# Optimization experiments

Hardware: AMD Instinct MI355X
Metric: run time of the kernel (lower is better)

## Reference

```python
import jax, jax.numpy as jnp
import numpy as np

F_NUM, KW, EMB = 256, 2, 300


def _conv_pool(X, W, b):
    # X: [B, L, E]; W: [F, kw, E]; b: [F]. Conv2d over [kw, E] window (full embedding
    # width) -> [B, F, T], ReLU, then AvgPool over the full T -> [B, F].
    kw = W.shape[1]
    T = X.shape[1] - kw + 1
    Xs = jnp.stack([X[:, k:k + T, :] for k in range(kw)], axis=1)  # [B, kw, T, E]
    y = jnp.einsum('fke,bkte->bft', W, Xs) + b[None, :, None]
    return jax.nn.relu(y).mean(axis=2)


def _unit(v):
    return v / jnp.sqrt((v * v).sum(-1, keepdims=True))


def setup_inputs() -> dict:
    key = jax.random.key(0)
    ks = jax.random.split(key, 20)
    wscale = 1.0 / np.sqrt(KW * EMB)
    inp = {
        'mention_vec': jax.random.normal(ks[0], (256, 10, 300), jnp.float32),
        'context_vec': jax.random.normal(ks[1], (256, 20, 300), jnp.float32),
        'doc_vec': jax.random.normal(ks[2], (200, 300), jnp.float32),
        'title_vec': jax.random.normal(ks[3], (1024, 20, 300), jnp.float32),
        'body_vec': jax.random.normal(ks[4], (1024, 200, 300), jnp.float32),
        'W_ms': jax.random.normal(ks[5], (F_NUM, KW, EMB), jnp.float32) * wscale,
        'b_ms': jax.random.normal(ks[6], (F_NUM,), jnp.float32) * wscale,
        'W_mc': jax.random.normal(ks[7], (F_NUM, KW, EMB), jnp.float32) * wscale,
        'b_mc': jax.random.normal(ks[8], (F_NUM,), jnp.float32) * wscale,
        'W_md': jax.random.normal(ks[9], (F_NUM, KW, EMB), jnp.float32) * wscale,
        'b_md': jax.random.normal(ks[10], (F_NUM,), jnp.float32) * wscale,
        'W_et': jax.random.normal(ks[11], (F_NUM, KW, EMB), jnp.float32) * wscale,
        'b_et': jax.random.normal(ks[12], (F_NUM,), jnp.float32) * wscale,
        'W_eb': jax.random.normal(ks[13], (F_NUM, KW, EMB), jnp.float32) * wscale,
        'b_eb': jax.random.normal(ks[14], (F_NUM,), jnp.float32) * wscale,
        'w_local': jax.random.normal(ks[15], (6,), jnp.float32) * 0.1,
        'b_local': jax.random.normal(ks[16], (1,), jnp.float32) * 0.1,
        'mention_entity': jax.random.randint(ks[17], (256, 1024), 0, 2, jnp.int32),
    }
    return inp


def reference(mention_vec, context_vec, doc_vec, title_vec, body_vec,
              W_ms, b_ms, W_mc, b_mc, W_md, b_md, W_et, b_et, W_eb, b_eb,
              w_local, b_local, mention_entity):
    # Per-branch conv + relu + avg-pool feature extraction -> [*, F] vectors.
    ms = _conv_pool(mention_vec, W_ms, b_ms)        # [m, F]
    mc = _conv_pool(context_vec, W_mc, b_mc)        # [m, F]
    md = _conv_pool(doc_vec[None], W_md, b_md)[0]   # [F]
    et = _conv_pool(title_vec, W_et, b_et)          # [n, F]
    eb = _conv_pool(body_vec, W_eb, b_eb)           # [n, F]

    nms, nmc, net, neb, nmd = _unit(ms), _unit(mc), _unit(et), _unit(eb), _unit(md)
    cos_st = nms @ net.T                             # [m, n]
    cos_ct = nmc @ net.T
    cos_sb = nms @ neb.T
    cos_cb = nmc @ neb.T
    cos_dt = jnp.broadcast_to((net @ nmd)[None, :], cos_st.shape)
    cos_db = jnp.broadcast_to((neb @ nmd)[None, :], cos_st.shape)

    # cos(x,y)/2 + 0.5, but features are exactly 0 where mention_entity == 0.
    feats = jnp.stack([cos_st, cos_dt, cos_ct, cos_sb, cos_db, cos_cb], axis=-1)
    feats = feats / 2.0 + 0.5                        # [m, n, 6]
    mask = mention_entity.astype(feats.dtype)
    feats = feats * mask[:, :, None]

    score = feats @ w_local + b_local[0]             # [m, n] (tiny 6->1 linear)
    score = score * mask

    # masked softmax with temperature 0.1 (e**(x/0.1) * mask, row-normalized)
    e = jnp.exp(score / 0.1) * mask
    norm = e / e.sum(axis=1, keepdims=True)
    return score, norm
```

## Files before the change

### kernel.cpp

```cpp
#include <hip/hip_runtime.h>
#include <math.h>

typedef __bf16 bf16_t;
typedef __bf16 bf16x4 __attribute__((ext_vector_type(4)));
typedef __bf16 bf16x8 __attribute__((ext_vector_type(8)));
typedef float  f32x4  __attribute__((ext_vector_type(4)));

#define FNUM 256
#define KPAD 608
#define NKS  19

#define BUFA_E 34200
#define BUFB_E 29120
#define GUARD_OFF 26400

__global__ __launch_bounds__(256)
void prep_w_swz(const float* __restrict__ w0, const float* __restrict__ w1,
                const float* __restrict__ w2, const float* __restrict__ w3,
                const float* __restrict__ w4, bf16_t* __restrict__ wp) {
    int tg = blockIdx.x * 4 + (threadIdx.x >> 6);
    if (tg >= 1520) return;
    int l  = threadIdx.x & 63;
    int br = tg / 304;
    int rem = tg % 304;
    int ks = rem / 16, ft = rem % 16;
    const float* src;
    switch (br) {
        case 0: src = w0; break;
        case 1: src = w1; break;
        case 2: src = w2; break;
        case 3: src = w3; break;
        default: src = w4; break;
    }
    int f = ft * 16 + (l & 15);
    int k0 = ks * 32 + (l >> 4) * 8;
    bf16x8 v;
#pragma unroll
    for (int e = 0; e < 8; e++) {
        int k = k0 + e;
        v[e] = (k < 600) ? (bf16_t)src[(size_t)f * 600 + k] : (bf16_t)0.f;
    }
    *(bf16x8*)(wp + (size_t)br * FNUM * KPAD + ((size_t)(ks * 16 + ft) * 512 + (size_t)l * 8)) = v;
}

template<int NFMAX>
__device__ __forceinline__ void kloop(const bf16_t* __restrict__ wa,
        const bf16_t* __restrict__ buf, f32x4 (&acc)[2][NFMAX],
        const int nf, const int (&boff)[NFMAX]) {
    bf16x8 aCur[2], aNxt[2];
    aCur[0] = *(const bf16x8*)(wa);
    aCur[1] = *(const bf16x8*)(wa + 512);
#pragma unroll
    for (int ks = 0; ks < NKS; ++ks) {
        if (ks + 1 < NKS) {
            const bf16_t* wn = wa + (size_t)(ks + 1) * (16 * 512);
            aNxt[0] = *(const bf16x8*)(wn);
            aNxt[1] = *(const bf16x8*)(wn + 512);
        }
        const int k0 = ks * 32;
#pragma unroll
        for (int j = 0; j < NFMAX; ++j) {
            if (j < nf) {
                const bf16_t* p = buf + boff[j] + k0;
                bf16x4 lo = *(const bf16x4*)(p);
                bf16x4 hi = *(const bf16x4*)(p + 4);
                bf16x8 bb = __builtin_shufflevector(lo, hi, 0, 1, 2, 3, 4, 5, 6, 7);
                acc[0][j] = __builtin_amdgcn_mfma_f32_16x16x32_bf16(aCur[0], bb, acc[0][j], 0, 0, 0);
                acc[1][j] = __builtin_amdgcn_mfma_f32_16x16x32_bf16(aCur[1], bb, acc[1][j], 0, 0, 0);
            }
        }
        aCur[0] = aNxt[0]; aCur[1] = aNxt[1];
    }
}

__device__ __forceinline__ void stage8(bf16_t* __restrict__ dst, const float* __restrict__ src,
                                       const int rows, const int lane256) {
    const float4* s4 = (const float4*)src;
    const int nv = rows * 75;
    for (int v0 = lane256; v0 < nv; v0 += 2048) {
        float4 t[8];
#pragma unroll
        for (int k = 0; k < 8; ++k) {
            int v = v0 + k * 256;
            if (v < nv) t[k] = s4[v];
        }
#pragma unroll
        for (int k = 0; k < 8; ++k) {
            int v = v0 + k * 256;
            if (v < nv) {
                bf16x4 h = { (bf16_t)t[k].x, (bf16_t)t[k].y, (bf16_t)t[k].z, (bf16_t)t[k].w };
                *(bf16x4*)(dst + (size_t)v * 4) = h;
            }
        }
    }
}

__global__ __launch_bounds__(768, 3)
void conv_body(const float* __restrict__ X, const bf16_t* __restrict__ Web,
               const float* __restrict__ beb, float* __restrict__ nebT,
               const float* __restrict__ Xdoc, const bf16_t* __restrict__ Wmd,
               const float* __restrict__ bmd, float* __restrict__ mdp) {
    __shared__ bf16_t bufA[BUFA_E];
    __shared__ bf16_t bufB[BUFB_E];
    __shared__ float feat[256];
    __shared__ float red[4];

    const int tid = threadIdx.x, l = tid & 63, w = tid >> 6, g = l >> 4, l15 = l & 15;
    const bool cons = (w < 8);
    const int bid = (int)blockIdx.x;
    const int nChunk = (bid >= 254) ? 9 : 8;

    auto chunkSrc = [&](int i, int& rows, int& nf, int& t0, bool& guard, bool& isDoc) -> const float* {
        int half;
        const float* base;
        if (i < 8) { int batch = bid * 4 + (i >> 1); half = i & 1; base = X + (size_t)batch * 60000; isDoc = false; }
        else       { half = bid - 254; base = Xdoc; isDoc = true; }
        rows = half ? 88 : 114; nf = half ? 6 : 7; t0 = half * 112; guard = (half != 0);
        return base + half * 33600;
    };

    if (!cons) {
        int rows, nf, t0; bool guard, isDoc;
        const float* s = chunkSrc(0, rows, nf, t0, guard, isDoc);
        stage8(bufA, s, rows, (w - 8) * 64 + l);
    }
    __syncthreads();

    float run[2][4];
    for (int i = 0; i < nChunk; ++i) {
        int rows, nf, t0; bool guard, isDoc;
        const float* src = chunkSrc(i, rows, nf, t0, guard, isDoc);
        (void)src; (void)rows; (void)guard;
        const bf16_t* buf = (i & 1) ? bufB : bufA;
        const bf16_t* Wb = isDoc ? Wmd : Web;
        const float* bp = isDoc ? bmd : beb;

        if (cons) {
            if ((i & 1) == 0) {
#pragma unroll
                for (int a = 0; a < 2; a++)
#pragma unroll
                    for (int r = 0; r < 4; r++) run[a][r] = 0.f;
            }
            int boff[7];
#pragma unroll
            for (int j = 0; j < 7; ++j) boff[j] = (j * 16 + l15) * 300 + g * 8;

            f32x4 acc[2][7];
#pragma unroll
            for (int a = 0; a < 2; a++)
#pragma unroll
                for (int j = 0; j < 7; j++) acc[a][j] = (f32x4){0.f, 0.f, 0.f, 0.f};

            const bf16_t* wa = Wb + (size_t)(2 * w) * 512 + (size_t)l * 8;
            kloop<7>(wa, buf, acc, nf, boff);

#pragma unroll
            for (int a = 0; a < 2; a++)
#pragma unroll
                for (int r = 0; r < 4; r++) {
                    const float bi = bp[32 * w + a * 16 + g * 4 + r];
                    float s = run[a][r];
#pragma unroll
                    for (int j = 0; j < 7; j++) {
                        if (j < nf) {
                            int t = t0 + j * 16 + l15;
                            float v = acc[a][j][r] + bi;
                            v = fmaxf(v, 0.f);
                            s += (t < 199) ? v : 0.f;
                        }
                    }
                    run[a][r] = s;
                }
        } else {
            if (i + 1 < nChunk) {
                int rows1, nf1, t01; bool guard1, isDoc1;
                const float* s1 = chunkSrc(i + 1, rows1, nf1, t01, guard1, isDoc1);
                bf16_t* nb = ((i + 1) & 1) ? bufB : bufA;
                const int lane256 = (w - 8) * 64 + l;
                stage8(nb, s1, rows1, lane256);
                if (guard1 && lane256 < 4) {
                    bf16x4 z = { (bf16_t)0.f, (bf16_t)0.f, (bf16_t)0.f, (bf16_t)0.f };
                    *(bf16x4*)(nb + GUARD_OFF + lane256 * 4) = z;
                }
            }
        }
        __syncthreads();

        const bool bEnd = (i == 8) || ((i & 1) == 1);
        if (bEnd) {
            if (cons) {
#pragma unroll
                for (int a = 0; a < 2; a++)
#pragma unroll
                    for (int r = 0; r < 4; r++) {
                        float s = run[a][r];
                        s += __shfl_xor(s, 1);
                        s += __shfl_xor(s, 2);
                        s += __shfl_xor(s, 4);
                        s += __shfl_xor(s, 8);
                        if (l15 == 0) feat[32 * w + a * 16 + g * 4 + r] = s;
                    }
            }
            __syncthreads();
            if (isDoc) {
                if (tid < 256) mdp[(size_t)(bid - 254) * 256 + tid] = feat[tid];
            } else {
                float v = 0.f, sq = 0.f;
                if (tid < 256) { v = feat[tid]; sq = v * v; }
                sq += __shfl_xor(sq, 1);
                sq += __shfl_xor(sq, 2);
                sq += __shfl_xor(sq, 4);
                sq += __shfl_xor(sq, 8);
                sq += __shfl_xor(sq, 16);
                sq += __shfl_xor(sq, 32);
                if (tid < 256 && l == 0) red[w] = sq;
                __syncthreads();
                if (tid < 256) {
                    float tot = red[0] + red[1] + red[2] + red[3];
                    int batch = bid * 4 + (i >> 1);
                    nebT[(size_t)tid * 1024 + batch] = v / sqrtf(tot);
                }
            }
        }
    }
}

template<int NFB, int L, int T, int BSTR, int ARRE>
__global__ __launch_bounds__(512, 4)
void conv_small(const float* __restrict__ XA, const bf16_t* __restrict__ WA,
                const float* __restrict__ bA, float* __restrict__ outA,
                const float* __restrict__ XB, const bf16_t* __restrict__ WB,
                const float* __restrict__ bB, float* __restrict__ outB,
                int nABlocks) {
    constexpr int NTOT = 4 * NFB;
    __shared__ bf16_t Xs[ARRE];
    __shared__ float feat4[4][256];

    const int tid = threadIdx.x, l = tid & 63, w = tid >> 6, g = l >> 4, l15 = l & 15;
    const bool modeA = ((int)blockIdx.x < nABlocks);
    const int grp = modeA ? (int)blockIdx.x : ((int)blockIdx.x - nABlocks);
    const int batch0 = grp * 4;
    const float* Xsrc = modeA ? XA : XB;
    const bf16_t* Wb = modeA ? WA : WB;
    const float* bp = modeA ? bA : bB;

#pragma unroll
    for (int b = 0; b < 4; ++b) {
        const float4* s4 = (const float4*)(Xsrc + (size_t)(batch0 + b) * (L * 300));
        for (int v = tid; v < L * 75; v += 512) {
            float4 f = s4[v];
            bf16x4 h = { (bf16_t)f.x, (bf16_t)f.y, (bf16_t)f.z, (bf16_t)f.w };
            *(bf16x4*)(Xs + b * BSTR + v * 4) = h;
        }
        if (tid < 2) {
            bf16x4 z = { (bf16_t)0.f, (bf16_t)0.f, (bf16_t)0.f, (bf16_t)0.f };
            *(bf16x4*)(Xs + b * BSTR + L * 300 + tid * 4) = z;
        }
    }
    __syncthreads();

    int boff[NTOT];
#pragma unroll
    for (int j = 0; j < NTOT; ++j)
        boff[j] = (j / NFB) * BSTR + ((j % NFB) * 16 + l15) * 300 + g * 8;

    f32x4 acc[2][NTOT];
#pragma unroll
    for (int a = 0; a < 2; a++)
#pragma unroll
        for (int j = 0; j < NTOT; j++) acc[a][j] = (f32x4){0.f, 0.f, 0.f, 0.f};

    const bf16_t* wa = Wb + (size_t)(2 * w) * 512 + (size_t)l * 8;
    kloop<NTOT>(wa, Xs, acc, NTOT, boff);

#pragma unroll
    for (int jb = 0; jb < 4; ++jb) {
#pragma unroll
        for (int a = 0; a < 2; a++)
#pragma unroll
            for (int r = 0; r < 4; r++) {
                const float bi = bp[32 * w + a * 16 + g * 4 + r];
                float s = 0.f;
#pragma unroll
                for (int jf = 0; jf < NFB; ++jf) {
                    int t = jf * 16 + l15;
                    float v = acc[a][jb * NFB + jf][r] + bi;
                    v = fmaxf(v, 0.f);
                    s += (t < T) ? v : 0.f;
                }
                s += __shfl_xor(s, 1);
                s += __shfl_xor(s, 2);
                s += __shfl_xor(s, 4);
                s += __shfl_xor(s, 8);
                if (l15 == 0) feat4[jb][32 * w + a * 16 + g * 4 + r] = s;
            }
    }
    __syncthreads();

    if (w < 4) {
        float vv[4];
        float sq = 0.f;
#pragma unroll
        for (int q = 0; q < 4; q++) { vv[q] = feat4[w][l * 4 + q]; sq += vv[q] * vv[q]; }
        sq += __shfl_xor(sq, 1);
        sq += __shfl_xor(sq, 2);
        sq += __shfl_xor(sq, 4);
        sq += __shfl_xor(sq, 8);
        sq += __shfl_xor(sq, 16);
        sq += __shfl_xor(sq, 32);
        float rsq = 1.f / sqrtf(sq);
        int batch = batch0 + w;
        if (modeA) {
#pragma unroll
            for (int q = 0; q < 4; q++)
                outA[(size_t)(l * 4 + q) * 1024 + batch] = vv[q] * rsq;
        } else {
            float4 o = { vv[0] * rsq, vv[1] * rsq, vv[2] * rsq, vv[3] * rsq };
            *(float4*)(outB + (size_t)batch * 256 + l * 4) = o;
        }
    }
}

__global__ __launch_bounds__(256)
void dt_db_kernel(const float* __restrict__ mdp, const float* __restrict__ netT,
                  const float* __restrict__ nebT, float* __restrict__ dt,
                  float* __restrict__ db) {
    __shared__ float md[256];
    __shared__ float red[4];
    int tid = threadIdx.x;
    float m = mdp[tid] + mdp[256 + tid];
    float sq = m * m;
    sq += __shfl_xor(sq, 1);
    sq += __shfl_xor(sq, 2);
    sq += __shfl_xor(sq, 4);
    sq += __shfl_xor(sq, 8);
    sq += __shfl_xor(sq, 16);
    sq += __shfl_xor(sq, 32);
    if ((tid & 63) == 0) red[tid >> 6] = sq;
    __syncthreads();
    float rn = 1.f / sqrtf(red[0] + red[1] + red[2] + red[3]);
    md[tid] = m * rn;
    __syncthreads();
    int n = blockIdx.x * 256 + tid;
    float dT = 0.f, dB = 0.f;
    for (int k = 0; k < 256; ++k) {
        float mk = md[k];
        dT += mk * netT[(size_t)k * 1024 + n];
        dB += mk * nebT[(size_t)k * 1024 + n];
    }
    dt[n] = dT;
    db[n] = dB;
}

__global__ __launch_bounds__(256)
void pair1(const float* __restrict__ nms, const float* __restrict__ nmc,
           const float* __restrict__ netT, const float* __restrict__ nebT,
           const float* __restrict__ dt, const float* __restrict__ db,
           const float* __restrict__ wl, const float* __restrict__ bl,
           const int* __restrict__ me, float* __restrict__ out,
           float* __restrict__ epart) {
    __shared__ float sA[4 * 256], sB[4 * 256];
    const int tid = threadIdx.x;
    const int mt = blockIdx.x >> 2;
    const int nt = blockIdx.x & 3;
    const int m0 = mt * 4, n0 = nt * 256;
    for (int v = tid; v < 1024; v += 256) {
        sA[v] = nms[(size_t)m0 * 256 + v];
        sB[v] = nmc[(size_t)m0 * 256 + v];
    }
    __syncthreads();
    const int ws = tid >> 6;
    const int nl = tid & 63;
    const int n  = n0 + nl * 4;
    const int m  = m0 + ws;

    float dst[4] = {0,0,0,0}, dct[4] = {0,0,0,0}, dsb[4] = {0,0,0,0}, dcb[4] = {0,0,0,0};
    for (int k = 0; k < 256; ++k) {
        float4 tv = *(const float4*)(netT + (size_t)k * 1024 + n);
        float4 bv = *(const float4*)(nebT + (size_t)k * 1024 + n);
        float a = sA[ws * 256 + k];
        float c = sB[ws * 256 + k];
        dst[0] += a * tv.x; dst[1] += a * tv.y; dst[2] += a * tv.z; dst[3] += a * tv.w;
        dct[0] += c * tv.x; dct[1] += c * tv.y; dct[2] += c * tv.z; dct[3] += c * tv.w;
        dsb[0] += a * bv.x; dsb[1] += a * bv.y; dsb[2] += a * bv.z; dsb[3] += a * bv.w;
        dcb[0] += c * bv.x; dcb[1] += c * bv.y; dcb[2] += c * bv.z; dcb[3] += c * bv.w;
    }

    float w0 = wl[0], w1 = wl[1], w2 = wl[2], w3 = wl[3], w4 = wl[4], w5 = wl[5], b = bl[0];
    float dtq[4], dbq[4];
    *(float4*)dtq = *(const float4*)(dt + n);
    *(float4*)dbq = *(const float4*)(db + n);
    const int* mp = me + (size_t)m * 1024 + n;
    float scv[4], evv[4];
    float esum = 0.f;
#pragma unroll
    for (int q = 0; q < 4; q++) {
        float msk = (float)mp[q];
        float f_st = dst[q] * 0.5f + 0.5f;
        float f_dt = dtq[q] * 0.5f + 0.5f;
        float f_ct = dct[q] * 0.5f + 0.5f;
        float f_sb = dsb[q] * 0.5f + 0.5f;
        float f_db = dbq[q] * 0.5f + 0.5f;
        float f_cb = dcb[q] * 0.5f + 0.5f;
        float s = f_st * w0 + f_dt * w1 + f_ct * w2 + f_sb * w3 + f_db * w4 + f_cb * w5 + b;
        s = (msk != 0.f) ? s : 0.f;
        scv[q] = s;
        evv[q] = (msk != 0.f) ? expf(s / 0.1f) : 0.f;
        esum += evv[q];
    }
    esum += __shfl_xor(esum, 1);
    esum += __shfl_xor(esum, 2);
    esum += __shfl_xor(esum, 4);
    esum += __shfl_xor(esum, 8);
    esum += __shfl_xor(esum, 16);
    esum += __shfl_xor(esum, 32);
    if (nl == 0) epart[(size_t)m * 4 + nt] = esum;

    *(float4*)(out + (size_t)m * 1024 + n) = *(float4*)scv;
    *(float4*)(out + 262144 + (size_t)m * 1024 + n) = *(float4*)evv;
}

__global__ __launch_bounds__(256)
void pair2(const float* __restrict__ epart, float* __restrict__ out2) {
    int m = blockIdx.x, tid = threadIdx.x;
    float tot = epart[(size_t)m * 4 + 0] + epart[(size_t)m * 4 + 1]
              + epart[(size_t)m * 4 + 2] + epart[(size_t)m * 4 + 3];
    float inv = 1.f / tot;
#pragma unroll
    for (int q = 0; q < 4; q++)
        out2[(size_t)m * 1024 + q * 256 + tid] *= inv;
}

extern "C" void kernel_launch(void* const* d_in, const int* in_sizes, int n_in,
                              void* d_out, int out_size, void* d_ws, size_t ws_size,
                              hipStream_t stream) {
    const float* mention = (const float*)d_in[0];
    const float* context = (const float*)d_in[1];
    const float* doc     = (const float*)d_in[2];
    const float* title   = (const float*)d_in[3];
    const float* body    = (const float*)d_in[4];
    const float* W_ms = (const float*)d_in[5];  const float* b_ms = (const float*)d_in[6];
    const float* W_mc = (const float*)d_in[7];  const float* b_mc = (const float*)d_in[8];
    const float* W_md = (const float*)d_in[9];  const float* b_md = (const float*)d_in[10];
    const float* W_et = (const float*)d_in[11]; const float* b_et = (const float*)d_in[12];
    const float* W_eb = (const float*)d_in[13]; const float* b_eb = (const float*)d_in[14];
    const float* w_local = (const float*)d_in[15];
    const float* b_local = (const float*)d_in[16];
    const int*   me      = (const int*)d_in[17];
    float* out = (float*)d_out;

    char* ws = (char*)d_ws;
    bf16_t* Wp = (bf16_t*)ws;
    size_t off = (size_t)5 * FNUM * KPAD * 2;
    float* nms  = (float*)(ws + off); off += 256 * 256 * 4;
    float* nmc  = (float*)(ws + off); off += 256 * 256 * 4;
    float* netT = (float*)(ws + off); off += 1024 * 256 * 4;
    float* nebT = (float*)(ws + off); off += 1024 * 256 * 4;
    float* mdp  = (float*)(ws + off); off += 2 * 256 * 4;
    float* dt   = (float*)(ws + off); off += 1024 * 4;
    float* db   = (float*)(ws + off); off += 1024 * 4;
    float* epart= (float*)(ws + off); off += 256 * 4 * 4;

    const bf16_t* Wms = Wp + (size_t)0 * FNUM * KPAD;
    const bf16_t* Wmc = Wp + (size_t)1 * FNUM * KPAD;
    const bf16_t* Wmd = Wp + (size_t)2 * FNUM * KPAD;
    const bf16_t* Wet = Wp + (size_t)3 * FNUM * KPAD;
    const bf16_t* Web = Wp + (size_t)4 * FNUM * KPAD;

    prep_w_swz<<<380, 256, 0, stream>>>(W_ms, W_mc, W_md, W_et, W_eb, Wp);

    conv_body<<<256, 768, 0, stream>>>(body, Web, b_eb, nebT, doc, Wmd, b_md, mdp);

    conv_small<2, 20, 19, 6016, 27968><<<320, 512, 0, stream>>>(
        title, Wet, b_et, netT, context, Wmc, b_mc, nmc, 256);
    conv_small<1, 10, 9, 5120, 20480><<<64, 512, 0, stream>>>(
        mention, Wms, b_ms, netT, mention, Wms, b_ms, nms, 0);

    dt_db_kernel<<<4, 256, 0, stream>>>(mdp, netT, nebT, dt, db);
    pair1<<<256, 256, 0, stream>>>(nms, nmc, netT, nebT, dt, db, w_local, b_local, me, out, epart);
    pair2<<<256, 256, 0, stream>>>(epart, out + 262144);
}
```

Baseline: 244.1 us.

## Split body conv into smaller time chunks with more, smaller-LDS blocks

Restructures the body conv kernel so each block handles two batches in five time chunks of up to 48 outputs, with much smaller LDS double buffers. The grid grows from 256 to 512 blocks and launch bounds request higher occupancy. The doc conv is now spread across five blocks, and the dt_db kernel sums five partial results. The trade-off is more chunk iterations, more barriers (including an added sync per batch end), and fewer MFMAs per LDS stage, in exchange for better latency hiding and more parallelism across CUs.

```diff
diff --git a/kernel.cpp b/kernel.cpp
--- a/kernel.cpp
+++ b/kernel.cpp
@@ -9,10 +9,8 @@
 #define FNUM 256
 #define KPAD 608
 #define NKS  19
-
-#define BUFA_E 34200
-#define BUFB_E 29120
-#define GUARD_OFF 26400
+#define BUF_E 14700
+#define BUF_G 14720
 
 __global__ __launch_bounds__(256)
 void prep_w_swz(const float* __restrict__ w0, const float* __restrict__ w1,
@@ -43,10 +41,9 @@
     *(bf16x8*)(wp + (size_t)br * FNUM * KPAD + ((size_t)(ks * 16 + ft) * 512 + (size_t)l * 8)) = v;
 }
 
-template<int NFMAX>
+template<int NF>
 __device__ __forceinline__ void kloop(const bf16_t* __restrict__ wa,
-        const bf16_t* __restrict__ buf, f32x4 (&acc)[2][NFMAX],
-        const int nf, const int (&boff)[NFMAX]) {
+        const bf16_t* __restrict__ buf, f32x4 (&acc)[2][NF], const int (&boff)[NF]) {
     bf16x8 aCur[2], aNxt[2];
     aCur[0] = *(const bf16x8*)(wa);
     aCur[1] = *(const bf16x8*)(wa + 512);
@@ -59,35 +56,63 @@
         }
         const int k0 = ks * 32;
 #pragma unroll
-        for (int j = 0; j < NFMAX; ++j) {
-            if (j < nf) {
-                const bf16_t* p = buf + boff[j] + k0;
-                bf16x4 lo = *(const bf16x4*)(p);
-                bf16x4 hi = *(const bf16x4*)(p + 4);
-                bf16x8 bb = __builtin_shufflevector(lo, hi, 0, 1, 2, 3, 4, 5, 6, 7);
-                acc[0][j] = __builtin_amdgcn_mfma_f32_16x16x32_bf16(aCur[0], bb, acc[0][j], 0, 0, 0);
-                acc[1][j] = __builtin_amdgcn_mfma_f32_16x16x32_bf16(aCur[1], bb, acc[1][j], 0, 0, 0);
-            }
+        for (int j = 0; j < NF; ++j) {
+            const bf16_t* p = buf + boff[j] + k0;
+            bf16x4 lo = *(const bf16x4*)(p);
+            bf16x4 hi = *(const bf16x4*)(p + 4);
+            bf16x8 bb = __builtin_shufflevector(lo, hi, 0, 1, 2, 3, 4, 5, 6, 7);
+            acc[0][j] = __builtin_amdgcn_mfma_f32_16x16x32_bf16(aCur[0], bb, acc[0][j], 0, 0, 0);
+            acc[1][j] = __builtin_amdgcn_mfma_f32_16x16x32_bf16(aCur[1], bb, acc[1][j], 0, 0, 0);
         }
         aCur[0] = aNxt[0]; aCur[1] = aNxt[1];
     }
 }
 
-__device__ __forceinline__ void stage8(bf16_t* __restrict__ dst, const float* __restrict__ src,
-                                       const int rows, const int lane256) {
+template<int NF>
+__device__ __forceinline__ void doChunk(const bf16_t* __restrict__ wa, const bf16_t* __restrict__ buf,
+        const float* __restrict__ bp, float (&run)[2][4], const int t0,
+        const int w, const int g, const int l15) {
+    const int bo = l15 * 300 + g * 8;
+    int boff[NF];
+#pragma unroll
+    for (int j = 0; j < NF; ++j) boff[j] = bo + j * 4800;
+    f32x4 acc[2][NF];
+#pragma unroll
+    for (int a = 0; a < 2; ++a)
+#pragma unroll
+        for (int j = 0; j < NF; ++j) acc[a][j] = (f32x4){0.f, 0.f, 0.f, 0.f};
+    kloop<NF>(wa, buf, acc, boff);
+#pragma unroll
+    for (int a = 0; a < 2; ++a)
+#pragma unroll
+        for (int r = 0; r < 4; ++r) {
+            const float bi = bp[32 * w + a * 16 + g * 4 + r];
+            float s = run[a][r];
+#pragma unroll
+            for (int j = 0; j < NF; ++j) {
+                int t = t0 + j * 16 + l15;
+                float v = acc[a][j][r] + bi;
+                v = fmaxf(v, 0.f);
+                s += (t < 199) ? v : 0.f;
+            }
+            run[a][r] = s;
+        }
+}
+
+__device__ __forceinline__ void stageN(bf16_t* __restrict__ dst, const float* __restrict__ src,
+                                       const int nF4, const int lane, const int stride) {
     const float4* s4 = (const float4*)src;
-    const int nv = rows * 75;
-    for (int v0 = lane256; v0 < nv; v0 += 2048) {
+    for (int v0 = lane; v0 < nF4; v0 += stride * 8) {
         float4 t[8];
 #pragma unroll
         for (int k = 0; k < 8; ++k) {
-            int v = v0 + k * 256;
-            if (v < nv) t[k] = s4[v];
+            int v = v0 + k * stride;
+            if (v < nF4) t[k] = s4[v];
         }
 #pragma unroll
         for (int k = 0; k < 8; ++k) {
-            int v = v0 + k * 256;
-            if (v < nv) {
+            int v = v0 + k * stride;
+            if (v < nF4) {
                 bf16x4 h = { (bf16_t)t[k].x, (bf16_t)t[k].y, (bf16_t)t[k].z, (bf16_t)t[k].w };
                 *(bf16x4*)(dst + (size_t)v * 4) = h;
             }
@@ -95,99 +120,71 @@
     }
 }
 
-__global__ __launch_bounds__(768, 3)
+__global__ __launch_bounds__(768, 8)
 void conv_body(const float* __restrict__ X, const bf16_t* __restrict__ Web,
                const float* __restrict__ beb, float* __restrict__ nebT,
                const float* __restrict__ Xdoc, const bf16_t* __restrict__ Wmd,
                const float* __restrict__ bmd, float* __restrict__ mdp) {
-    __shared__ bf16_t bufA[BUFA_E];
-    __shared__ bf16_t bufB[BUFB_E];
+    __shared__ bf16_t bufA[BUF_G];
+    __shared__ bf16_t bufB[BUF_G];
     __shared__ float feat[256];
     __shared__ float red[4];
 
     const int tid = threadIdx.x, l = tid & 63, w = tid >> 6, g = l >> 4, l15 = l & 15;
     const bool cons = (w < 8);
     const int bid = (int)blockIdx.x;
-    const int nChunk = (bid >= 254) ? 9 : 8;
-
-    auto chunkSrc = [&](int i, int& rows, int& nf, int& t0, bool& guard, bool& isDoc) -> const float* {
-        int half;
-        const float* base;
-        if (i < 8) { int batch = bid * 4 + (i >> 1); half = i & 1; base = X + (size_t)batch * 60000; isDoc = false; }
-        else       { half = bid - 254; base = Xdoc; isDoc = true; }
-        rows = half ? 88 : 114; nf = half ? 6 : 7; t0 = half * 112; guard = (half != 0);
-        return base + half * 33600;
+    const int nChunk = (bid < 5) ? 11 : 10;
+
+    if (tid < 8) bufA[BUF_E + tid] = (bf16_t)0.f;
+    else if (tid < 16) bufB[BUF_E + (tid - 8)] = (bf16_t)0.f;
+
+    auto desc = [&](int i, int& nf, int& t0, int& rows, bool& isDoc, int& batch) -> const float* {
+        int c;
+        if (i < 10) { batch = bid * 2 + (i >= 5 ? 1 : 0); c = (i >= 5) ? (i - 5) : i; isDoc = false; }
+        else        { batch = -1; c = bid; isDoc = true; }
+        nf   = (c < 4) ? 3 : 1;
+        rows = (c < 4) ? 49 : 8;
+        t0   = 48 * c;
+        const float* base = isDoc ? Xdoc : (X + (size_t)batch * 60000);
+        return base + (size_t)t0 * 300;
     };
 
-    if (!cons) {
-        int rows, nf, t0; bool guard, isDoc;
-        const float* s = chunkSrc(0, rows, nf, t0, guard, isDoc);
-        stage8(bufA, s, rows, (w - 8) * 64 + l);
+    {
+        int nf, t0, rows, ba; bool d;
+        const float* s = desc(0, nf, t0, rows, d, ba);
+        stageN(bufA, s, rows * 75, tid, 768);
     }
     __syncthreads();
 
     float run[2][4];
     for (int i = 0; i < nChunk; ++i) {
-        int rows, nf, t0; bool guard, isDoc;
-        const float* src = chunkSrc(i, rows, nf, t0, guard, isDoc);
-        (void)src; (void)rows; (void)guard;
-        const bf16_t* buf = (i & 1) ? bufB : bufA;
+        int nf, t0, rows, batch; bool isDoc;
+        desc(i, nf, t0, rows, isDoc, batch);
+        bf16_t* buf = (i & 1) ? bufB : bufA;
         const bf16_t* Wb = isDoc ? Wmd : Web;
         const float* bp = isDoc ? bmd : beb;
 
         if (cons) {
-            if ((i & 1) == 0) {
+            if (i == 0 || i == 5 || i == 10) {
 #pragma unroll
                 for (int a = 0; a < 2; a++)
 #pragma unroll
                     for (int r = 0; r < 4; r++) run[a][r] = 0.f;
             }
-            int boff[7];
-#pragma unroll
-            for (int j = 0; j < 7; ++j) boff[j] = (j * 16 + l15) * 300 + g * 8;
-
-            f32x4 acc[2][7];
-#pragma unroll
-            for (int a = 0; a < 2; a++)
-#pragma unroll
-                for (int j = 0; j < 7; j++) acc[a][j] = (f32x4){0.f, 0.f, 0.f, 0.f};
-
             const bf16_t* wa = Wb + (size_t)(2 * w) * 512 + (size_t)l * 8;
-            kloop<7>(wa, buf, acc, nf, boff);
-
-#pragma unroll
-            for (int a = 0; a < 2; a++)
-#pragma unroll
-                for (int r = 0; r < 4; r++) {
-                    const float bi = bp[32 * w + a * 16 + g * 4 + r];
-                    float s = run[a][r];
-#pragma unroll
-                    for (int j = 0; j < 7; j++) {
-                        if (j < nf) {
-                            int t = t0 + j * 16 + l15;
-                            float v = acc[a][j][r] + bi;
-                            v = fmaxf(v, 0.f);
-                            s += (t < 199) ? v : 0.f;
-                        }
-                    }
-                    run[a][r] = s;
-                }
+            if (nf == 3) doChunk<3>(wa, buf, bp, run, t0, w, g, l15);
+            else         doChunk<1>(wa, buf, bp, run, t0, w, g, l15);
         } else {
             if (i + 1 < nChunk) {
-                int rows1, nf1, t01; bool guard1, isDoc1;
-                const float* s1 = chunkSrc(i + 1, rows1, nf1, t01, guard1, isDoc1);
+                int nf1, t01, rows1, ba1; bool d1;
+                const float* s1 = desc(i + 1, nf1, t01, rows1, d1, ba1);
                 bf16_t* nb = ((i + 1) & 1) ? bufB : bufA;
-                const int lane256 = (w - 8) * 64 + l;
-                stage8(nb, s1, rows1, lane256);
-                if (guard1 && lane256 < 4) {
-                    bf16x4 z = { (bf16_t)0.f, (bf16_t)0.f, (bf16_t)0.f, (bf16_t)0.f };
-                    *(bf16x4*)(nb + GUARD_OFF + lane256 * 4) = z;
-                }
+                stageN(nb, s1, rows1 * 75, (w - 8) * 64 + l, 256);
             }
         }
         __syncthreads();
 
-        const bool bEnd = (i == 8) || ((i & 1) == 1);
+        const bool bEnd = (i == 4) || (i == 9) || (i == 10);
         if (bEnd) {
             if (cons) {
 #pragma unroll
@@ -204,7 +201,7 @@
             }
             __syncthreads();
             if (isDoc) {
-                if (tid < 256) mdp[(size_t)(bid - 254) * 256 + tid] = feat[tid];
+                if (tid < 256) mdp[(size_t)bid * 256 + tid] = feat[tid];
             } else {
                 float v = 0.f, sq = 0.f;
                 if (tid < 256) { v = feat[tid]; sq = v * v; }
@@ -218,10 +215,10 @@
                 __syncthreads();
                 if (tid < 256) {
                     float tot = red[0] + red[1] + red[2] + red[3];
-                    int batch = bid * 4 + (i >> 1);
                     nebT[(size_t)tid * 1024 + batch] = v / sqrtf(tot);
                 }
             }
+            __syncthreads();
         }
     }
 }
@@ -272,7 +269,7 @@
         for (int j = 0; j < NTOT; j++) acc[a][j] = (f32x4){0.f, 0.f, 0.f, 0.f};
 
     const bf16_t* wa = Wb + (size_t)(2 * w) * 512 + (size_t)l * 8;
-    kloop<NTOT>(wa, Xs, acc, NTOT, boff);
+    kloop<NTOT>(wa, Xs, acc, boff);
 
 #pragma unroll
     for (int jb = 0; jb < 4; ++jb) {
@@ -329,7 +326,9 @@
     __shared__ float md[256];
     __shared__ float red[4];
     int tid = threadIdx.x;
-    float m = mdp[tid] + mdp[256 + tid];
+    float m = 0.f;
+#pragma unroll
+    for (int c = 0; c < 5; ++c) m += mdp[c * 256 + tid];
     float sq = m * m;
     sq += __shfl_xor(sq, 1);
     sq += __shfl_xor(sq, 2);
@@ -457,7 +456,7 @@
     float* nmc  = (float*)(ws + off); off += 256 * 256 * 4;
     float* netT = (float*)(ws + off); off += 1024 * 256 * 4;
     float* nebT = (float*)(ws + off); off += 1024 * 256 * 4;
-    float* mdp  = (float*)(ws + off); off += 2 * 256 * 4;
+    float* mdp  = (float*)(ws + off); off += 5 * 256 * 4;
     float* dt   = (float*)(ws + off); off += 1024 * 4;
     float* db   = (float*)(ws + off); off += 1024 * 4;
     float* epart= (float*)(ws + off); off += 256 * 4 * 4;
@@ -470,7 +469,7 @@
 
     prep_w_swz<<<380, 256, 0, stream>>>(W_ms, W_mc, W_md, W_et, W_eb, Wp);
 
-    conv_body<<<256, 768, 0, stream>>>(body, Web, b_eb, nebT, doc, Wmd, b_md, mdp);
+    conv_body<<<512, 768, 0, stream>>>(body, Web, b_eb, nebT, doc, Wmd, b_md, mdp);
 
     conv_small<2, 20, 19, 6016, 27968><<<320, 512, 0, stream>>>(
         title, Wet, b_et, netT, context, Wmc, b_mc, nmc, 256);
```

Measured after the change: 271.4 us. 11.2% more time.
